# Optimization experiments

Hardware: AMD Instinct MI355X
Metric: run time of the kernel (lower is better)

The kernel has to match this reference:

```python
import jax, jax.numpy as jnp
import numpy as np

# LIF neuron constants (the CUDA kernel source is not shipped; these are the
# standard fused SNN semantics documented for this layer)
V_DECAY = 0.9       # membrane leak per step
V_THRESH = 1.0      # spike threshold
REFRAC_PERIOD = 5.0 # refractory timer reset value (in steps)

B_SZ, SEQ, HID, STATE = 8, 4096, 1024, 64


def setup_inputs() -> dict:
    key = jax.random.key(0)
    k1, k2, k3, k4, k5 = jax.random.split(key, 5)
    return {
        "input": jax.random.normal(k1, (B_SZ, SEQ, HID), dtype=jnp.float32),
        "ssm_A": jax.random.normal(k2, (STATE, STATE), dtype=jnp.float32) * 0.01,
        "ssm_B": jax.random.normal(k3, (STATE, 1), dtype=jnp.float32) * 0.1,
        "ssm_C": jax.random.normal(k4, (1, STATE), dtype=jnp.float32) * 0.1,
        "ssm_D": jax.random.normal(k5, (1, 1), dtype=jnp.float32) * 0.01,
    }


def reference(input, ssm_A, ssm_B, ssm_C, ssm_D):
    batch, seq_len, hidden = input.shape
    state = ssm_A.shape[0]

    # initial states (module.forward always starts from zeros)
    v0 = jnp.zeros((batch, hidden), dtype=jnp.float32)
    r0 = jnp.zeros((batch, hidden), dtype=jnp.float32)
    h0 = jnp.zeros((batch, state), dtype=jnp.float32)

    Bvec = ssm_B[:, 0]      # [state]
    Cvec = ssm_C[0, :]      # [state]
    Dsc = ssm_D[0, 0]       # scalar

    def step(carry, x_t):
        v, r, h = carry
        # --- SNN membrane + refractory update ---
        v = v * V_DECAY + x_t
        active = r <= 0.0
        spike = jnp.where(active & (v >= V_THRESH), 1.0, 0.0)  # [B,H]
        v = jnp.where(spike > 0.0, 0.0, v)
        r = jnp.where(spike > 0.0, REFRAC_PERIOD, jnp.maximum(r - 1.0, 0.0))
        # --- SSM recurrence, driven by pooled spike rate (scalar per batch) ---
        u = jnp.mean(spike, axis=-1)                 # [B]
        h = jnp.einsum('ns,bs->bn', ssm_A, h) + u[:, None] * Bvec  # [B,N]
        y = h @ Cvec + Dsc * u                       # [B]
        out_t = spike + y[:, None]                   # [B,H]
        return (v, r, h), out_t

    xs = jnp.swapaxes(input, 0, 1)                   # [S,B,H]
    _, ys = jax.lax.scan(step, (v0, r0, h0), xs)
    return jnp.swapaxes(ys, 0, 1)                    # [B,S,H]
```

## Files before the change

### kernel.cpp

```cpp
#include <hip/hip_runtime.h>
#include <cstdint>
#include <cstddef>

#define B_SZ   8
#define SEQ    4096
#define HID    1024
#define NCH    8
#define CHUNK  512
#define WARM   256
#define JTAP   16
#define TS     32

typedef float vfloat4 __attribute__((ext_vector_type(4)));

__device__ __forceinline__ void snn_step(float& v, float& r, float xv, bool& s) {
  v = __fadd_rn(__fmul_rn(v, 0.9f), xv);
  s = (r <= 0.0f) && (v >= 1.0f);
  v = s ? 0.0f : v;
  r = s ? 5.0f : fmaxf(r - 1.0f, 0.0f);
}

__device__ __forceinline__ void proc32_emit(const float* xv, float& v, float& r, int lane,
                                            unsigned long long* __restrict__ sp, int t) {
  unsigned long long my = 0;
  #pragma unroll
  for (int k = 0; k < 32; ++k) {
    bool s; snn_step(v, r, xv[k], s);
    unsigned long long m = __ballot(s);
    my = ((lane & 31) == k) ? m : my;
  }
  if (lane < 32) sp[t + lane] = my;
}

__device__ __forceinline__ void proc32_warm(const float* xv, float& v, float& r) {
  #pragma unroll
  for (int k = 0; k < 32; ++k) { bool s; snn_step(v, r, xv[k], s); }
}

__global__ __launch_bounds__(256) void snn_kernel(const float* __restrict__ x,
                                                  unsigned long long* __restrict__ spk) {
  const int hid  = blockIdx.x * 256 + threadIdx.x;
  const int b    = blockIdx.y;
  const int c    = blockIdx.z;
  const int lane = threadIdx.x & 63;
  const int wv   = hid >> 6;
  const int t0   = c * CHUNK;
  const int t1   = t0 + CHUNK;
  const int tw   = (t0 >= WARM) ? (t0 - WARM) : 0;
  const float* __restrict__ xp = x + (size_t)(b * SEQ) * HID + hid;
  unsigned long long* __restrict__ sp = spk + (size_t)(b * 16 + wv) * SEQ;

  float v = 0.0f, r = 0.0f;
  float xa[32], xb[32];

  #pragma unroll
  for (int k = 0; k < 32; ++k) xa[k] = xp[(size_t)(tw + k) * HID];

  for (int t = tw; t < t1; t += 64) {
    #pragma unroll
    for (int k = 0; k < 32; ++k) xb[k] = xp[(size_t)(t + 32 + k) * HID];

    if (t >= t0) proc32_emit(xa, v, r, lane, sp, t);
    else         proc32_warm(xa, v, r);

    if (t + 64 < t1) {
      #pragma unroll
      for (int k = 0; k < 32; ++k) xa[k] = xp[(size_t)(t + 64 + k) * HID];
    }

    if (t + 32 >= t0) proc32_emit(xb, v, r, lane, sp, t + 32);
    else              proc32_warm(xb, v, r);
  }
}

__global__ __launch_bounds__(256) void yout_kernel(const unsigned long long* __restrict__ spk,
                                                   const float* __restrict__ A,
                                                   const float* __restrict__ Bv,
                                                   const float* __restrict__ Cv,
                                                   const float* __restrict__ Dp,
                                                   vfloat4* __restrict__ out) {
  __shared__ unsigned long long lm[16][TS + JTAP];
  __shared__ float ws[JTAP];
  __shared__ float su[TS + JTAP];
  __shared__ float sy[TS];

  const int tid = threadIdx.x;
  const int b   = blockIdx.y;
  const int t0  = blockIdx.x * TS;
  const unsigned long long* __restrict__ sb = spk + (size_t)b * 16 * SEQ;

  if (tid < 64) {
    const int lane = tid;
    float arow[64];
    #pragma unroll 8
    for (int s2 = 0; s2 < 64; ++s2) arow[s2] = A[lane * 64 + s2];
    float p = Bv[lane];
    const float cv = Cv[lane];
    for (int m = 0; m < JTAP; ++m) {
      float t = cv * p;
      #pragma unroll
      for (int off = 32; off; off >>= 1) t += __shfl_xor(t, off);
      if (lane == 0) ws[m] = t;
      float n0 = 0.f, n1 = 0.f, n2 = 0.f, n3 = 0.f;
      #pragma unroll
      for (int s2 = 0; s2 < 64; s2 += 4) {
        n0 = fmaf(arow[s2 + 0], __shfl(p, s2 + 0), n0);
        n1 = fmaf(arow[s2 + 1], __shfl(p, s2 + 1), n1);
        n2 = fmaf(arow[s2 + 2], __shfl(p, s2 + 2), n2);
        n3 = fmaf(arow[s2 + 3], __shfl(p, s2 + 3), n3);
      }
      p = (n0 + n1) + (n2 + n3);
    }
  } else {
    const int i = tid - 64;
    if (i < TS + JTAP) {
      const int t = t0 - JTAP + i;
      #pragma unroll
      for (int wv = 0; wv < 16; ++wv)
        lm[wv][i] = (t >= 0) ? sb[(size_t)wv * SEQ + t] : 0ull;
    }
  }
  __syncthreads();

  if (tid < TS + JTAP) {
    int cc = 0;
    #pragma unroll
    for (int wv = 0; wv < 16; ++wv) cc += __popcll(lm[wv][tid]);
    su[tid] = cc * (1.0f / 1024.0f);
  }
  __syncthreads();

  if (tid < TS) {
    float acc = Dp[0] * su[JTAP + tid];
    #pragma unroll
    for (int m = 0; m < JTAP; ++m) acc = fmaf(ws[m], su[JTAP + tid - m], acc);
    sy[tid] = acc;
  }
  __syncthreads();

  const int wv = tid >> 4;
  const int sh = (tid & 15) * 4;
  vfloat4* op = out + (size_t)(b * SEQ + t0) * 256 + tid;
  #pragma unroll 8
  for (int j = 0; j < TS; ++j) {
    const unsigned long long m = lm[wv][JTAP + j];
    const float yv = sy[j];
    vfloat4 o;
    o.x = ((m >> (sh + 0)) & 1ull) ? 1.0f + yv : yv;
    o.y = ((m >> (sh + 1)) & 1ull) ? 1.0f + yv : yv;
    o.z = ((m >> (sh + 2)) & 1ull) ? 1.0f + yv : yv;
    o.w = ((m >> (sh + 3)) & 1ull) ? 1.0f + yv : yv;
    __builtin_nontemporal_store(o, &op[(size_t)j * 256]);
  }
}

extern "C" void kernel_launch(void* const* d_in, const int* in_sizes, int n_in,
                              void* d_out, int out_size, void* d_ws, size_t ws_size,
                              hipStream_t stream) {
  const float* x  = (const float*)d_in[0];
  const float* A  = (const float*)d_in[1];
  const float* Bv = (const float*)d_in[2];
  const float* Cv = (const float*)d_in[3];
  const float* Dp = (const float*)d_in[4];

  unsigned long long* spk = (unsigned long long*)d_ws;

  dim3 g1(HID / 256, B_SZ, NCH);
  snn_kernel<<<g1, 256, 0, stream>>>(x, spk);

  dim3 g2(SEQ / TS, B_SZ);
  yout_kernel<<<g2, 256, 0, stream>>>(spk, A, Bv, Cv, Dp, (vfloat4*)d_out);
}
```

Measured before the change: 283.2 us.

## Stage SNN input through double-buffered LDS via async global-to-LDS loads

Rewrites the spike kernel to load 32-timestep tiles of the input into a double-buffered LDS tile using global_load_lds 16-byte async copies, replacing the per-thread strided register loads. Blocks shrink to 128 threads covering 128 hidden units, and the sequence split goes from 8 chunks to 4 larger chunks, which cuts the redundant warm-up recompute. The cost is fewer blocks in flight, since the grid becomes 8x8x4 with 2 waves each, plus a block barrier every tile. The async loads also assume the LDS destination layout matches the wave-level address pattern.

```diff
diff --git a/kernel.cpp b/kernel.cpp
--- a/kernel.cpp
+++ b/kernel.cpp
@@ -5,11 +5,13 @@
 #define B_SZ   8
 #define SEQ    4096
 #define HID    1024
-#define NCH    8
-#define CHUNK  512
+#define NCH    4
+#define CHUNK  1024
 #define WARM   256
 #define JTAP   16
 #define TS     32
+#define TT     32
+#define HB     128
 
 typedef float vfloat4 __attribute__((ext_vector_type(4)));
 
@@ -20,56 +22,77 @@
   r = s ? 5.0f : fmaxf(r - 1.0f, 0.0f);
 }
 
-__device__ __forceinline__ void proc32_emit(const float* xv, float& v, float& r, int lane,
-                                            unsigned long long* __restrict__ sp, int t) {
-  unsigned long long my = 0;
-  #pragma unroll
-  for (int k = 0; k < 32; ++k) {
-    bool s; snn_step(v, r, xv[k], s);
-    unsigned long long m = __ballot(s);
-    my = ((lane & 31) == k) ? m : my;
-  }
-  if (lane < 32) sp[t + lane] = my;
+__device__ __forceinline__ void async_ld16(const float* g, float* l) {
+  __builtin_amdgcn_global_load_lds((const __attribute__((address_space(1))) void*)g,
+                                   (__attribute__((address_space(3))) void*)l,
+                                   16, 0, 0);
 }
 
-__device__ __forceinline__ void proc32_warm(const float* xv, float& v, float& r) {
-  #pragma unroll
-  for (int k = 0; k < 32; ++k) { bool s; snn_step(v, r, xv[k], s); }
-}
-
-__global__ __launch_bounds__(256) void snn_kernel(const float* __restrict__ x,
+__global__ __launch_bounds__(128) void snn_kernel(const float* __restrict__ x,
                                                   unsigned long long* __restrict__ spk) {
-  const int hid  = blockIdx.x * 256 + threadIdx.x;
+  __shared__ float tile[2][TT][HB];
+  const int tid  = threadIdx.x;
+  const int lane = tid & 63;
+  const int w    = tid >> 6;
+  const int hb   = blockIdx.x;
   const int b    = blockIdx.y;
   const int c    = blockIdx.z;
-  const int lane = threadIdx.x & 63;
-  const int wv   = hid >> 6;
   const int t0   = c * CHUNK;
-  const int t1   = t0 + CHUNK;
-  const int tw   = (t0 >= WARM) ? (t0 - WARM) : 0;
-  const float* __restrict__ xp = x + (size_t)(b * SEQ) * HID + hid;
+  const int tw   = (c == 0) ? 0 : (t0 - WARM);
+  const int nt   = (t0 + CHUNK - tw) / TT;
+  const float* __restrict__ gbase = x + (size_t)(b * SEQ) * HID + hb * HB;
+  const int wv = hb * 2 + w;
   unsigned long long* __restrict__ sp = spk + (size_t)(b * 16 + wv) * SEQ;
 
+  const size_t goff = (size_t)(lane >> 5) * HID + (size_t)(lane & 31) * 4;
+
+  {
+    const float* g0 = gbase + (size_t)tw * HID + goff;
+    float* l0 = &tile[0][0][0];
+    #pragma unroll
+    for (int p = 0; p < 8; ++p)
+      async_ld16(g0 + (size_t)(w * 16 + 2 * p) * HID, l0 + (w * 8 + p) * 256);
+  }
+
   float v = 0.0f, r = 0.0f;
-  float xa[32], xb[32];
+  for (int i = 0; i < nt; ++i) {
+    __syncthreads();
+    const int tt = tw + i * TT;
 
-  #pragma unroll
-  for (int k = 0; k < 32; ++k) xa[k] = xp[(size_t)(tw + k) * HID];
-
-  for (int t = tw; t < t1; t += 64) {
-    #pragma unroll
-    for (int k = 0; k < 32; ++k) xb[k] = xp[(size_t)(t + 32 + k) * HID];
-
-    if (t >= t0) proc32_emit(xa, v, r, lane, sp, t);
-    else         proc32_warm(xa, v, r);
-
-    if (t + 64 < t1) {
+    if (i + 1 < nt) {
+      const float* g = gbase + (size_t)(tt + TT) * HID + goff;
+      float* l = &tile[(i + 1) & 1][0][0];
       #pragma unroll
-      for (int k = 0; k < 32; ++k) xa[k] = xp[(size_t)(t + 64 + k) * HID];
+      for (int p = 0; p < 8; ++p)
+        async_ld16(g + (size_t)(w * 16 + 2 * p) * HID, l + (w * 8 + p) * 256);
     }
 
-    if (t + 32 >= t0) proc32_emit(xb, v, r, lane, sp, t + 32);
-    else              proc32_warm(xb, v, r);
+    const float (*tl)[HB] = tile[i & 1];
+    if (tt >= t0) {
+      unsigned long long my = 0;
+      #pragma unroll
+      for (int g8 = 0; g8 < 4; ++g8) {
+        float xv[8];
+        #pragma unroll
+        for (int k = 0; k < 8; ++k) xv[k] = tl[g8 * 8 + k][tid];
+        #pragma unroll
+        for (int k = 0; k < 8; ++k) {
+          bool s; snn_step(v, r, xv[k], s);
+          unsigned long long m = __ballot(s);
+          my = ((lane & 31) == (g8 * 8 + k)) ? m : my;
+        }
+      }
+      if (lane < 32) sp[tt + lane] = my;
+    } else {
+      #pragma unroll
+      for (int g8 = 0; g8 < 4; ++g8) {
+        float xv[8];
+        #pragma unroll
+        for (int k = 0; k < 8; ++k) xv[k] = tl[g8 * 8 + k][tid];
+        #pragma unroll
+        for (int k = 0; k < 8; ++k) { bool s; snn_step(v, r, xv[k], s); }
+      }
+    }
   }
 }
 
@@ -165,8 +188,8 @@
 
   unsigned long long* spk = (unsigned long long*)d_ws;
 
-  dim3 g1(HID / 256, B_SZ, NCH);
-  snn_kernel<<<g1, 256, 0, stream>>>(x, spk);
+  dim3 g1(HID / HB, B_SZ, NCH);
+  snn_kernel<<<g1, 128, 0, stream>>>(x, spk);
 
   dim3 g2(SEQ / TS, B_SZ);
   yout_kernel<<<g2, 256, 0, stream>>>(spk, A, Bv, Cv, Dp, (vfloat4*)d_out);
```

After: 288.1 us. No clear change (+1.7%).
